# Performance work log

Hardware: AMD Instinct MI355X
Metric: run time of the kernel (lower is better)

Reference implementation:

```python
import jax, jax.numpy as jnp
import numpy as np

DT = 0.01
EPS = 1e-5


def setup_inputs() -> dict:
    key = jax.random.key(0)
    ks = jax.random.split(key, 20)
    B, H, IN, COV, CH, OH, OUT = 1024, 64, 8, 16, 64, 128, 2
    NE, OPE = 400, 256            # events, observations per event
    TOT = NE * OPE

    def w(k, sh, sc=0.05):
        return jax.random.normal(k, sh, dtype=jnp.float32) * sc

    return {
        'time_uniq': jnp.arange(NE, dtype=jnp.float32) * DT,   # event k fires at grid step k
        'time_ptr': jnp.arange(NE + 1, dtype=jnp.int32) * OPE,  # uniform obs per event
        'X': jax.random.normal(ks[0], (TOT, IN), dtype=jnp.float32),
        'sample_ids': jax.random.randint(ks[1], (TOT,), 0, B, dtype=jnp.int32),
        'covs': jax.random.normal(ks[2], (B, COV), dtype=jnp.float32),
        'T': 5,
        'cov_W1': w(ks[3], (CH, COV)), 'cov_b1': jnp.zeros((CH,), jnp.float32),
        'cov_W2': w(ks[4], (H, CH)),   'cov_b2': jnp.zeros((H,), jnp.float32),
        'gb_Wih': w(ks[5], (3 * H, IN)), 'gb_Whh': w(ks[6], (3 * H, H)),
        'gb_bih': jnp.zeros((3 * H,), jnp.float32), 'gb_bhh': jnp.zeros((3 * H,), jnp.float32),
        'gx_W': w(ks[7], (3 * H, 1)), 'gx_b': jnp.zeros((3 * H,), jnp.float32),
        'ghr_W': w(ks[8], (H, H)), 'ghz_W': w(ks[9], (H, H)), 'ghh_W': w(ks[10], (H, H)),
        'out_W1': w(ks[11], (OH, H)), 'out_b1': jnp.zeros((OH,), jnp.float32),
        'out_W2': w(ks[12], (OUT, OH)), 'out_b2': jnp.zeros((OUT,), jnp.float32),
    }


def _forward(time_uniq, time_ptr, X, sample_ids, covs, T,
             cov_W1, cov_b1, cov_W2, cov_b2,
             gb_Wih, gb_Whh, gb_bih, gb_bhh,
             gx_W, gx_b, ghr_W, ghz_W, ghh_W,
             out_W1, out_b1, out_W2, out_b2):
    n_events = time_uniq.shape[0]
    ope = X.shape[0] // n_events          # uniform observations per event (static)
    n_steps = int(round(T / DT))
    delta_t = DT

    # covariates_map (dropout p=0 -> identity)
    h0 = jnp.tanh(jnp.maximum(covs @ cov_W1.T + cov_b1, 0.0) @ cov_W2.T + cov_b2)

    def gru_bayes(x, h):                  # torch.nn.GRUCell semantics (gates r,z,n)
        gi = x @ gb_Wih.T + gb_bih
        gh = h @ gb_Whh.T + gb_bhh
        ir, iz, inn = jnp.split(gi, 3, axis=1)
        hr, hz, hn = jnp.split(gh, 3, axis=1)
        r = jax.nn.sigmoid(ir + hr)
        z = jax.nn.sigmoid(iz + hz)
        n = jnp.tanh(inn + r * hn)
        return (1.0 - z) * n + z * h

    def gru_ode(h):                       # FullGRUODECell with x = zeros
        px = jnp.zeros((h.shape[0], 1), h.dtype)
        gx = px @ gx_W.T + gx_b
        xr, xz, xh = jnp.split(gx, 3, axis=1)
        r = jax.nn.sigmoid(xr + h @ ghr_W.T)
        z = jax.nn.sigmoid(xz + h @ ghz_W.T)
        u = jnp.tanh(xh + (r * h) @ ghh_W.T)
        return h + delta_t * (1.0 - z) * (u - h)

    times = jnp.arange(n_steps, dtype=jnp.float32) * DT
    offs = jnp.arange(ope)

    def step(carry, t):
        h, i = carry
        ic = jnp.minimum(i, n_events - 1)
        fire = (i < n_events) & (time_uniq[ic] <= t + EPS)   # <=1 event per grid step
        obs = time_ptr[ic] + offs
        idx = sample_ids[obs]
        h_upd = h.at[idx].set(gru_bayes(X[obs], h[idx]))
        h = jnp.where(fire, h_upd, h)
        i = i + fire.astype(i.dtype)
        h_rec = h                          # recorded after events, before ODE step
        h = gru_ode(h)
        return (h, i), h_rec

    (h_last, _), h_steps = jax.lax.scan(step, (h0, jnp.int32(0)), times)
    h_path = jnp.concatenate([h_steps, h_last[None]], axis=0)   # [n_steps+1, B, H]

    # net_out (dropout p=0 -> identity)
    o = jnp.maximum(jnp.einsum('tbh,oh->tbo', h_path, out_W1) + out_b1, 0.0)
    return jnp.einsum('tbh,oh->tbo', o, out_W2) + out_b2


def reference(time_uniq, time_ptr, X, sample_ids, covs, T,
              cov_W1, cov_b1, cov_W2, cov_b2,
              gb_Wih, gb_Whh, gb_bih, gb_bhh,
              gx_W, gx_b, ghr_W, ghz_W, ghh_W,
              out_W1, out_b1, out_W2, out_b2):
    return _forward(time_uniq, time_ptr, X, sample_ids, covs, T,
                    cov_W1, cov_b1, cov_W2, cov_b2,
                    gb_Wih, gb_Whh, gb_bih, gb_bhh,
                    gx_W, gx_b, ghr_W, ghz_W, ghh_W,
                    out_W1, out_b1, out_W2, out_b2)
```

## Files before the change

### kernel.cpp

```cpp
#include <hip/hip_runtime.h>

#define DT_F 0.01f
#define EPS_F 1e-5f
#define NEG_INF_I (-1073741824)
#define NEC 1024

typedef _Float16 f16;
typedef _Float16 f16x2 __attribute__((ext_vector_type(2)));
typedef _Float16 f16x8 __attribute__((ext_vector_type(8)));
typedef float f32x4 __attribute__((ext_vector_type(4)));

#define MFMA16(a, b, c) __builtin_amdgcn_mfma_f32_16x16x32_f16((a), (b), (c), 0, 0, 0)

__device__ __forceinline__ float rl(float v, int l) {
  return __int_as_float(__builtin_amdgcn_readlane(__float_as_int(v), l));
}
__device__ __forceinline__ float sigm(float x) {
  float e = __builtin_amdgcn_exp2f(-1.442695041f * x);
  return __builtin_amdgcn_rcpf(1.0f + e);
}
__device__ __forceinline__ float tanhf_fast(float x) {
  float e = __builtin_amdgcn_exp2f(2.885390082f * x);
  return fmaf(-2.0f, __builtin_amdgcn_rcpf(e + 1.0f), 1.0f);
}
__device__ __forceinline__ float dot2(unsigned w, unsigned h, float acc) {
  return __builtin_amdgcn_fdot2(__builtin_bit_cast(f16x2, w),
                                __builtin_bit_cast(f16x2, h), acc, false);
}
__device__ __forceinline__ unsigned packf16(float a, float b) {
  return __builtin_bit_cast(unsigned, __builtin_amdgcn_cvt_pkrtz(a, b));
}
#define ANCH4(v) asm volatile("" : "+v"((v).x), "+v"((v).y), "+v"((v).z), "+v"((v).w))

__global__ void build_evtab_kernel(const int* __restrict__ sample_ids,
                                   const int* __restrict__ time_ptr,
                                   int* __restrict__ evtabT, int B, int ope) {
  int k = blockIdx.x;
  int base = time_ptr[k];
  for (int t = threadIdx.x; t < ope; t += blockDim.x) {
    int obs = base + t;
    int sid = sample_ids[obs];
    atomicMax(&evtabT[(long)sid * NEC + k], obs + 1);
  }
}

__global__ void pack_pairs_kernel(const float* __restrict__ ghr,
                                  const float* __restrict__ ghz,
                                  const float* __restrict__ ghh,
                                  const float* __restrict__ gbWhh,
                                  const float* __restrict__ gbWih,
                                  unsigned* __restrict__ odeP,
                                  unsigned* __restrict__ bayP,
                                  unsigned* __restrict__ wihP, int IN) {
  int idx = blockIdx.x * 256 + threadIdx.x;
  if (idx < 3 * 64 * 32) {
    int p = idx & 31, r = idx >> 5;
    int g = r >> 6, i = r & 63;
    const float* src = (g == 0) ? ghr : ((g == 1) ? ghz : ghh);
    odeP[idx] = packf16(src[i * 64 + 2 * p], src[i * 64 + 2 * p + 1]);
    bayP[idx] = packf16(gbWhh[r * 64 + 2 * p], gbWhh[r * 64 + 2 * p + 1]);
  }
  if (idx < 3 * 64 * 4) {
    int p = idx & 3, r = idx >> 2;
    float a = (2 * p < IN) ? gbWih[r * IN + 2 * p] : 0.0f;
    float b = (2 * p + 1 < IN) ? gbWih[r * IN + 2 * p + 1] : 0.0f;
    wihP[idx] = packf16(a, b);
  }
}

__global__ void pack_head_kernel(const float* __restrict__ W1, f16* __restrict__ w1P) {
  int f = blockIdx.x;
  int l = threadIdx.x;
  int t = f >> 1, kf = f & 1;
  int n = 16 * t + (l & 15);
  for (int j = 0; j < 8; ++j) {
    int k = 8 * (l >> 4) + j + 32 * kf;
    w1P[f * 512 + l * 8 + j] = (f16)W1[n * 64 + k];
  }
}

__global__ __launch_bounds__(128, 2) void evolve_kernel(
    const float* __restrict__ time_uniq,
    const float* __restrict__ X,
    const float* __restrict__ covs,
    const float* __restrict__ cov_W1, const float* __restrict__ cov_b1,
    const float* __restrict__ cov_W2, const float* __restrict__ cov_b2,
    const float* __restrict__ gb_bih, const float* __restrict__ gb_bhh,
    const float* __restrict__ gx_b,
    const unsigned* __restrict__ odeP, const unsigned* __restrict__ bayP,
    const unsigned* __restrict__ wihP,
    const int* __restrict__ evtabT,
    f16* __restrict__ hp16,
    int B, int NE, int n_steps, int IN, int COV)
{
  __shared__ unsigned sBW[3 * 64 * 32];
  __shared__ int sStep[1024];
  __shared__ int sEvt[1024];
  __shared__ __align__(16) f16 sHimg[64];
  __shared__ __align__(16) f16 sRHimg[64];

  const int tid = threadIdx.x;
  const int wid = tid >> 6, lane = tid & 63;
  const int b = blockIdx.x;
  const int necap = (NE < NEC) ? NE : NEC;

  for (int idx = tid; idx < 3 * 64 * 32; idx += 128) {
    int c = idx & 31, r = idx >> 5;
    int i = r & 63, s = c >> 2;
    sBW[r * 32 + (((s ^ (i & 7)) << 2) | (c & 3))] = bayP[idx];
  }
  for (int e = tid; e < necap; e += 128)
    sEvt[e] = evtabT[(long)b * NEC + e];
  if (wid == 0) {
    int pm = NEG_INF_I;
    int loc[16];
#pragma unroll
    for (int j = 0; j < 16; ++j) {
      int e = lane * 16 + j;
      int gv = NEG_INF_I;
      if (e < necap) {
        float tu = time_uniq[e];
        int k0 = (int)floorf((tu - EPS_F) * 100.0f) - 2;
        if (k0 < 0) k0 = 0;
        while ((float)k0 * DT_F + EPS_F < tu) ++k0;
        gv = k0 - e;
      }
      pm = max(pm, gv);
      loc[j] = pm;
    }
    int tot = pm;
#pragma unroll
    for (int off = 1; off < 64; off <<= 1) {
      int v = __shfl_up(tot, off);
      if (lane >= off) tot = max(tot, v);
    }
    int excl = __shfl_up(tot, 1);
    if (lane == 0) excl = NEG_INF_I;
#pragma unroll
    for (int j = 0; j < 16; ++j)
      sStep[lane * 16 + j] = lane * 16 + j + max(loc[j], excl);
  }
  if (wid == 0) {
    float cacc = cov_b1[lane];
    for (int c = 0; c < COV; ++c)
      cacc = fmaf(covs[b * COV + c], cov_W1[lane * COV + c], cacc);
    float cl = fmaxf(cacc, 0.0f);
    float hacc = cov_b2[lane];
#pragma unroll
    for (int j = 0; j < 64; ++j)
      hacc = fmaf(rl(cl, j), cov_W2[lane * 64 + j], hacc);
    sHimg[lane] = (f16)tanhf_fast(hacc);
  }
  __syncthreads();

  const uint4* odeQ = (const uint4*)odeP;
  const uint4* hq4 = (const uint4*)sHimg;
  const uint4* rq4 = (const uint4*)sRHimg;

  if (wid == 0) {
    uint4 WZ[8], WU[8];
#pragma unroll
    for (int q = 0; q < 8; ++q) {
      WZ[q] = odeQ[(1 * 64 + lane) * 8 + q];
      WU[q] = odeQ[(2 * 64 + lane) * 8 + q];
    }
#pragma unroll
    for (int q = 0; q < 8; ++q) { ANCH4(WZ[q]); ANCH4(WU[q]); }
    const uint4* wihQ = (const uint4*)wihP;

    const float xz = gx_b[64 + lane], xh = gx_b[128 + lane];
    const float crz_r = gb_bih[lane] + gb_bhh[lane];
    const float crz_z = gb_bih[64 + lane] + gb_bhh[64 + lane];
    const float bihn = gb_bih[128 + lane], bhhn = gb_bhh[128 + lane];

    float h = (float)sHimg[lane];

    int e_next = 0, s_next = 0x7fffffff, v_cur = 0, v_pipe = 0;
    float xf[8];
#pragma unroll
    for (int kk = 0; kk < 8; ++kk) xf[kk] = 0.0f;
    if (necap > 0) {
      s_next = sStep[0];
      v_cur = sEvt[0];
      if (v_cur > 0) {
        const float* xp = X + (long)(v_cur - 1) * IN;
#pragma unroll
        for (int kk = 0; kk < 8; ++kk) xf[kk] = (kk < IN) ? xp[kk] : 0.0f;
      }
      v_pipe = (necap > 1) ? sEvt[1] : 0;
    }

#pragma unroll 1
    for (int k = 0; k < n_steps; ++k) {
      if (k == s_next) {
        const bool fire = (v_cur > 0);
        if (fire) {
          unsigned xp0 = packf16(xf[0], xf[1]), xp1 = packf16(xf[2], xf[3]);
          unsigned xp2 = packf16(xf[4], xf[5]), xp3 = packf16(xf[6], xf[7]);
          uint4 wxr = wihQ[lane], wxz = wihQ[64 + lane], wxn = wihQ[128 + lane];
          float ar = crz_r, az = crz_z, anh = bhhn, ani = bihn;
          ar = dot2(wxr.x, xp0, ar); ar = dot2(wxr.y, xp1, ar);
          ar = dot2(wxr.z, xp2, ar); ar = dot2(wxr.w, xp3, ar);
          az = dot2(wxz.x, xp0, az); az = dot2(wxz.y, xp1, az);
          az = dot2(wxz.z, xp2, az); az = dot2(wxz.w, xp3, az);
          ani = dot2(wxn.x, xp0, ani); ani = dot2(wxn.y, xp1, ani);
          ani = dot2(wxn.z, xp2, ani); ani = dot2(wxn.w, xp3, ani);
          float ar1 = 0.f, az1 = 0.f, an1 = 0.f;
#pragma unroll
          for (int q = 0; q < 8; ++q) {
            uint4 hh = hq4[q];
            int sw = ((q ^ (lane & 7)) << 2);
            uint4 br = *(const uint4*)&sBW[(0 * 64 + lane) * 32 + sw];
            uint4 bz = *(const uint4*)&sBW[(1 * 64 + lane) * 32 + sw];
            uint4 bn = *(const uint4*)&sBW[(2 * 64 + lane) * 32 + sw];
            ar  = dot2(br.x, hh.x, ar);   ar1 = dot2(br.y, hh.y, ar1);
            ar  = dot2(br.z, hh.z, ar);   ar1 = dot2(br.w, hh.w, ar1);
            az  = dot2(bz.x, hh.x, az);   az1 = dot2(bz.y, hh.y, az1);
            az  = dot2(bz.z, hh.z, az);   az1 = dot2(bz.w, hh.w, az1);
            anh = dot2(bn.x, hh.x, anh);  an1 = dot2(bn.y, hh.y, an1);
            anh = dot2(bn.z, hh.z, anh);  an1 = dot2(bn.w, hh.w, an1);
          }
          float r = sigm(ar + ar1);
          float z = sigm(az + az1);
          float n = tanhf_fast(ani + r * (anh + an1));
          h = (1.0f - z) * n + z * h;
          sHimg[lane] = (f16)h;
        }
        ++e_next;
        if (e_next < necap) {
          s_next = sStep[e_next];
          v_cur = v_pipe;
          if (v_cur > 0) {
            const float* xp = X + (long)(v_cur - 1) * IN;
#pragma unroll
            for (int kk = 0; kk < 8; ++kk) xf[kk] = (kk < IN) ? xp[kk] : 0.0f;
          }
          v_pipe = (e_next + 1 < necap) ? sEvt[e_next + 1] : 0;
        } else {
          s_next = 0x7fffffff;
          v_cur = 0;
        }
        if (fire) __syncthreads();
      }

      float az0 = xz, az1 = 0.f, az2 = 0.f, az3 = 0.f;
#pragma unroll
      for (int q = 0; q < 8; ++q) {
        uint4 hp = hq4[q];
        az0 = dot2(WZ[q].x, hp.x, az0); az1 = dot2(WZ[q].y, hp.y, az1);
        az2 = dot2(WZ[q].z, hp.z, az2); az3 = dot2(WZ[q].w, hp.w, az3);
      }
      float z = sigm((az0 + az1) + (az2 + az3));
      __syncthreads();

      float au0 = xh, au1 = 0.f, au2 = 0.f, au3 = 0.f;
#pragma unroll
      for (int q = 0; q < 8; ++q) {
        uint4 rp = rq4[q];
        au0 = dot2(WU[q].x, rp.x, au0); au1 = dot2(WU[q].y, rp.y, au1);
        au2 = dot2(WU[q].z, rp.z, au2); au3 = dot2(WU[q].w, rp.w, au3);
      }
      float u = tanhf_fast((au0 + au1) + (au2 + au3));
      h = fmaf(DT_F * (1.0f - z), u - h, h);
      sHimg[lane] = (f16)h;
      __syncthreads();
    }
  } else {
    uint4 WR[8];
#pragma unroll
    for (int q = 0; q < 8; ++q) WR[q] = odeQ[(0 * 64 + lane) * 8 + q];
#pragma unroll
    for (int q = 0; q < 8; ++q) ANCH4(WR[q]);
    const float xr = gx_b[lane];

    f16* hps = hp16 + (long)b * 64 + lane;
    const long rowstride = (long)B * 64;

    int e_next = 0, s_next = 0x7fffffff, v_cur = 0, v_pipe = 0;
    if (necap > 0) {
      s_next = sStep[0];
      v_cur = sEvt[0];
      v_pipe = (necap > 1) ? sEvt[1] : 0;
    }

#pragma unroll 1
    for (int k = 0; k < n_steps; ++k) {
      if (k == s_next) {
        const bool fire = (v_cur > 0);
        ++e_next;
        if (e_next < necap) {
          s_next = sStep[e_next];
          v_cur = v_pipe;
          v_pipe = (e_next + 1 < necap) ? sEvt[e_next + 1] : 0;
        } else {
          s_next = 0x7fffffff;
          v_cur = 0;
        }
        if (fire) __syncthreads();
      }

      f16 hraw = sHimg[lane];
      *hps = hraw;
      hps += rowstride;
      float hf = (float)hraw;

      float ar0 = xr, ar1 = 0.f, ar2 = 0.f, ar3 = 0.f;
#pragma unroll
      for (int q = 0; q < 8; ++q) {
        uint4 hp = hq4[q];
        ar0 = dot2(WR[q].x, hp.x, ar0); ar1 = dot2(WR[q].y, hp.y, ar1);
        ar2 = dot2(WR[q].z, hp.z, ar2); ar3 = dot2(WR[q].w, hp.w, ar3);
      }
      float r = sigm((ar0 + ar1) + (ar2 + ar3));
      sRHimg[lane] = (f16)(r * hf);
      __syncthreads();
      __syncthreads();
    }
    *hps = sHimg[lane];
  }
}

__global__ __launch_bounds__(256, 4) void head_mfma_kernel(
    const f16* __restrict__ hp16, const f16* __restrict__ w1P,
    const float* __restrict__ b1, const float* __restrict__ W2,
    const float* __restrict__ b2, float* __restrict__ out, long nrows)
{
  const int wq = threadIdx.x >> 6, lane = threadIdx.x & 63;
  const int col = lane & 15;
  const long rowbase = ((long)blockIdx.x * 4 + wq) * 64;

  f16x8 Wf[8][2];
#pragma unroll
  for (int t = 0; t < 8; ++t)
#pragma unroll
    for (int kf = 0; kf < 2; ++kf)
      Wf[t][kf] = ((const f16x8*)w1P)[(2 * t + kf) * 64 + lane];

  float b1v[8], w2a[8], w2b[8];
#pragma unroll
  for (int t = 0; t < 8; ++t) {
    b1v[t] = b1[16 * t + col];
    w2a[t] = W2[16 * t + col];
    w2b[t] = W2[128 + 16 * t + col];
  }
  const float b20 = b2[0], b21 = b2[1];

#pragma unroll 1
  for (int g = 0; g < 4; ++g) {
    long row0 = rowbase + g * 16;
    long arow = row0 + col;
    f16x8 aH0 = {0, 0, 0, 0, 0, 0, 0, 0}, aH1 = aH0;
    if (arow < nrows) {
      const f16x8* ap = (const f16x8*)(hp16 + arow * 64);
      aH0 = ap[lane >> 4];
      aH1 = ap[(lane >> 4) + 4];
    }
    float p0[4] = {0.f, 0.f, 0.f, 0.f}, p1[4] = {0.f, 0.f, 0.f, 0.f};
#pragma unroll
    for (int t = 0; t < 8; ++t) {
      f32x4 c = {0.f, 0.f, 0.f, 0.f};
      c = MFMA16(aH0, Wf[t][0], c);
      c = MFMA16(aH1, Wf[t][1], c);
#pragma unroll
      for (int i = 0; i < 4; ++i) {
        float o = fmaxf(c[i] + b1v[t], 0.0f);
        p0[i] = fmaf(o, w2a[t], p0[i]);
        p1[i] = fmaf(o, w2b[t], p1[i]);
      }
    }
#pragma unroll
    for (int off = 1; off < 16; off <<= 1) {
#pragma unroll
      for (int i = 0; i < 4; ++i) {
        p0[i] += __shfl_xor(p0[i], off);
        p1[i] += __shfl_xor(p1[i], off);
      }
    }
    if (col == 0) {
#pragma unroll
      for (int i = 0; i < 4; ++i) {
        long row = row0 + (lane >> 4) * 4 + i;
        if (row < nrows) {
          out[row * 2 + 0] = p0[i] + b20;
          out[row * 2 + 1] = p1[i] + b21;
        }
      }
    }
  }
}

extern "C" void kernel_launch(void* const* d_in, const int* in_sizes, int n_in,
                              void* d_out, int out_size, void* d_ws, size_t ws_size,
                              hipStream_t stream) {
  const float* time_uniq  = (const float*)d_in[0];
  const int*   time_ptr   = (const int*)d_in[1];
  const float* X          = (const float*)d_in[2];
  const int*   sample_ids = (const int*)d_in[3];
  const float* covs       = (const float*)d_in[4];
  const float* cov_W1     = (const float*)d_in[6];
  const float* cov_b1     = (const float*)d_in[7];
  const float* cov_W2     = (const float*)d_in[8];
  const float* cov_b2     = (const float*)d_in[9];
  const float* gb_Wih     = (const float*)d_in[10];
  const float* gb_Whh     = (const float*)d_in[11];
  const float* gb_bih     = (const float*)d_in[12];
  const float* gb_bhh     = (const float*)d_in[13];
  const float* gx_b       = (const float*)d_in[15];
  const float* ghr_W      = (const float*)d_in[16];
  const float* ghz_W      = (const float*)d_in[17];
  const float* ghh_W      = (const float*)d_in[18];
  const float* out_W1     = (const float*)d_in[19];
  const float* out_b1     = (const float*)d_in[20];
  const float* out_W2     = (const float*)d_in[21];
  const float* out_b2     = (const float*)d_in[22];

  int NE   = in_sizes[0];
  int TOT  = in_sizes[3];
  int IN   = in_sizes[2] / TOT;
  int CH   = in_sizes[7];
  int COV  = in_sizes[6] / CH;
  int B    = in_sizes[4] / COV;
  int OUTD = in_sizes[22];
  int n_steps = out_size / (B * OUTD) - 1;
  int OPE  = TOT / NE;

  char* ws = (char*)d_ws;
  int* evtabT = (int*)ws;
  size_t evbytes = (size_t)B * NEC * sizeof(int);
  size_t off1 = (evbytes + 255) & ~(size_t)255;
  unsigned* odeP = (unsigned*)(ws + off1);
  unsigned* bayP = odeP + 3 * 64 * 32;
  unsigned* wihP = bayP + 3 * 64 * 32;
  size_t off2 = off1 + (((3 * 64 * 32 * 2 + 3 * 64 * 4) * sizeof(unsigned) + 255) & ~(size_t)255);
  f16* w1P = (f16*)(ws + off2);
  size_t off3 = off2 + ((16 * 512 * sizeof(f16) + 255) & ~(size_t)255);
  f16* hp16 = (f16*)(ws + off3);

  hipMemsetAsync(evtabT, 0, evbytes, stream);
  build_evtab_kernel<<<NE, 256, 0, stream>>>(sample_ids, time_ptr, evtabT, B, OPE);
  pack_pairs_kernel<<<24, 256, 0, stream>>>(ghr_W, ghz_W, ghh_W, gb_Whh, gb_Wih,
                                            odeP, bayP, wihP, IN);
  pack_head_kernel<<<16, 64, 0, stream>>>(out_W1, w1P);
  evolve_kernel<<<B, 128, 0, stream>>>(
      time_uniq, X, covs, cov_W1, cov_b1, cov_W2, cov_b2,
      gb_bih, gb_bhh, gx_b, odeP, bayP, wihP,
      evtabT, hp16, B, NE, n_steps, IN, COV);
  long nrows = (long)(n_steps + 1) * B;
  int hb = (int)((nrows + 255) / 256);
  head_mfma_kernel<<<hb, 256, 0, stream>>>(hp16, w1P, out_b1, out_W2, out_b2,
                                           (float*)d_out, nrows);
}
```

Measured before the change: 432.5 us.

## Move reset gate onto main wave and offload update gate to helper wave

Wave 0 now computes the ODE reset gate and r*h itself, then runs the candidate matvec straight away. Because the write to sRHimg and the read that follows happen in the same wavefront, no cross-wave barrier is needed between them. The update gate z moves to the helper wave and is passed back through a new shared array, so it is off the serial r→u dependency chain. The hidden-state vector is also kept in registers (hpre) after each update instead of being reloaded from LDS, and wave 0 raises its scheduling priority. One side effect is that r*h now uses the fp32 h rather than its f16-rounded value, which slightly changes the numerics.

```diff
diff --git a/kernel.cpp b/kernel.cpp
--- a/kernel.cpp
+++ b/kernel.cpp
@@ -98,6 +98,7 @@
   __shared__ int sEvt[1024];
   __shared__ __align__(16) f16 sHimg[64];
   __shared__ __align__(16) f16 sRHimg[64];
+  __shared__ float sZ[64];
 
   const int tid = threadIdx.x;
   const int wid = tid >> 6, lane = tid & 63;
@@ -158,22 +159,26 @@
   const uint4* rq4 = (const uint4*)sRHimg;
 
   if (wid == 0) {
-    uint4 WZ[8], WU[8];
+    __builtin_amdgcn_s_setprio(1);
+    uint4 WR[8], WU[8];
 #pragma unroll
     for (int q = 0; q < 8; ++q) {
-      WZ[q] = odeQ[(1 * 64 + lane) * 8 + q];
+      WR[q] = odeQ[(0 * 64 + lane) * 8 + q];
       WU[q] = odeQ[(2 * 64 + lane) * 8 + q];
     }
 #pragma unroll
-    for (int q = 0; q < 8; ++q) { ANCH4(WZ[q]); ANCH4(WU[q]); }
+    for (int q = 0; q < 8; ++q) { ANCH4(WR[q]); ANCH4(WU[q]); }
     const uint4* wihQ = (const uint4*)wihP;
 
-    const float xz = gx_b[64 + lane], xh = gx_b[128 + lane];
+    const float xr = gx_b[lane], xh = gx_b[128 + lane];
     const float crz_r = gb_bih[lane] + gb_bhh[lane];
     const float crz_z = gb_bih[64 + lane] + gb_bhh[64 + lane];
     const float bihn = gb_bih[128 + lane], bhhn = gb_bhh[128 + lane];
 
     float h = (float)sHimg[lane];
+    uint4 hpre[8];
+#pragma unroll
+    for (int q = 0; q < 8; ++q) hpre[q] = hq4[q];
 
     int e_next = 0, s_next = 0x7fffffff, v_cur = 0, v_pipe = 0;
     float xf[8];
@@ -208,23 +213,24 @@
           float ar1 = 0.f, az1 = 0.f, an1 = 0.f;
 #pragma unroll
           for (int q = 0; q < 8; ++q) {
-            uint4 hh = hq4[q];
             int sw = ((q ^ (lane & 7)) << 2);
             uint4 br = *(const uint4*)&sBW[(0 * 64 + lane) * 32 + sw];
             uint4 bz = *(const uint4*)&sBW[(1 * 64 + lane) * 32 + sw];
             uint4 bn = *(const uint4*)&sBW[(2 * 64 + lane) * 32 + sw];
-            ar  = dot2(br.x, hh.x, ar);   ar1 = dot2(br.y, hh.y, ar1);
-            ar  = dot2(br.z, hh.z, ar);   ar1 = dot2(br.w, hh.w, ar1);
-            az  = dot2(bz.x, hh.x, az);   az1 = dot2(bz.y, hh.y, az1);
-            az  = dot2(bz.z, hh.z, az);   az1 = dot2(bz.w, hh.w, az1);
-            anh = dot2(bn.x, hh.x, anh);  an1 = dot2(bn.y, hh.y, an1);
-            anh = dot2(bn.z, hh.z, anh);  an1 = dot2(bn.w, hh.w, an1);
+            ar  = dot2(br.x, hpre[q].x, ar);   ar1 = dot2(br.y, hpre[q].y, ar1);
+            ar  = dot2(br.z, hpre[q].z, ar);   ar1 = dot2(br.w, hpre[q].w, ar1);
+            az  = dot2(bz.x, hpre[q].x, az);   az1 = dot2(bz.y, hpre[q].y, az1);
+            az  = dot2(bz.z, hpre[q].z, az);   az1 = dot2(bz.w, hpre[q].w, az1);
+            anh = dot2(bn.x, hpre[q].x, anh);  an1 = dot2(bn.y, hpre[q].y, an1);
+            anh = dot2(bn.z, hpre[q].z, anh);  an1 = dot2(bn.w, hpre[q].w, an1);
           }
           float r = sigm(ar + ar1);
           float z = sigm(az + az1);
           float n = tanhf_fast(ani + r * (anh + an1));
           h = (1.0f - z) * n + z * h;
           sHimg[lane] = (f16)h;
+#pragma unroll
+          for (int q = 0; q < 8; ++q) hpre[q] = hq4[q];
         }
         ++e_next;
         if (e_next < necap) {
@@ -243,16 +249,15 @@
         if (fire) __syncthreads();
       }
 
-      float az0 = xz, az1 = 0.f, az2 = 0.f, az3 = 0.f;
+      float ar0 = xr, ar1 = 0.f, ar2 = 0.f, ar3 = 0.f;
 #pragma unroll
       for (int q = 0; q < 8; ++q) {
-        uint4 hp = hq4[q];
-        az0 = dot2(WZ[q].x, hp.x, az0); az1 = dot2(WZ[q].y, hp.y, az1);
-        az2 = dot2(WZ[q].z, hp.z, az2); az3 = dot2(WZ[q].w, hp.w, az3);
-      }
-      float z = sigm((az0 + az1) + (az2 + az3));
-      __syncthreads();
-
+        ar0 = dot2(WR[q].x, hpre[q].x, ar0); ar1 = dot2(WR[q].y, hpre[q].y, ar1);
+        ar2 = dot2(WR[q].z, hpre[q].z, ar2); ar3 = dot2(WR[q].w, hpre[q].w, ar3);
+      }
+      float r = sigm((ar0 + ar1) + (ar2 + ar3));
+
+      sRHimg[lane] = (f16)(r * h);
       float au0 = xh, au1 = 0.f, au2 = 0.f, au3 = 0.f;
 #pragma unroll
       for (int q = 0; q < 8; ++q) {
@@ -260,18 +265,22 @@
         au0 = dot2(WU[q].x, rp.x, au0); au1 = dot2(WU[q].y, rp.y, au1);
         au2 = dot2(WU[q].z, rp.z, au2); au3 = dot2(WU[q].w, rp.w, au3);
       }
+      __syncthreads();
+      float zv = sZ[lane];
       float u = tanhf_fast((au0 + au1) + (au2 + au3));
-      h = fmaf(DT_F * (1.0f - z), u - h, h);
+      h = fmaf(DT_F * (1.0f - zv), u - h, h);
       sHimg[lane] = (f16)h;
+#pragma unroll
+      for (int q = 0; q < 8; ++q) hpre[q] = hq4[q];
       __syncthreads();
     }
   } else {
-    uint4 WR[8];
-#pragma unroll
-    for (int q = 0; q < 8; ++q) WR[q] = odeQ[(0 * 64 + lane) * 8 + q];
-#pragma unroll
-    for (int q = 0; q < 8; ++q) ANCH4(WR[q]);
-    const float xr = gx_b[lane];
+    uint4 WZ[8];
+#pragma unroll
+    for (int q = 0; q < 8; ++q) WZ[q] = odeQ[(1 * 64 + lane) * 8 + q];
+#pragma unroll
+    for (int q = 0; q < 8; ++q) ANCH4(WZ[q]);
+    const float xz = gx_b[64 + lane];
 
     f16* hps = hp16 + (long)b * 64 + lane;
     const long rowstride = (long)B * 64;
@@ -302,17 +311,15 @@
       f16 hraw = sHimg[lane];
       *hps = hraw;
       hps += rowstride;
-      float hf = (float)hraw;
-
-      float ar0 = xr, ar1 = 0.f, ar2 = 0.f, ar3 = 0.f;
+
+      float az0 = xz, az1 = 0.f, az2 = 0.f, az3 = 0.f;
 #pragma unroll
       for (int q = 0; q < 8; ++q) {
-        uint4 hp = hq4[q];
-        ar0 = dot2(WR[q].x, hp.x, ar0); ar1 = dot2(WR[q].y, hp.y, ar1);
-        ar2 = dot2(WR[q].z, hp.z, ar2); ar3 = dot2(WR[q].w, hp.w, ar3);
-      }
-      float r = sigm((ar0 + ar1) + (ar2 + ar3));
-      sRHimg[lane] = (f16)(r * hf);
+        uint4 hh = hq4[q];
+        az0 = dot2(WZ[q].x, hh.x, az0); az1 = dot2(WZ[q].y, hh.y, az1);
+        az2 = dot2(WZ[q].z, hh.z, az2); az3 = dot2(WZ[q].w, hh.w, az3);
+      }
+      sZ[lane] = sigm((az0 + az1) + (az2 + az3));
       __syncthreads();
       __syncthreads();
     }
```

Result: slower. 441.2 us (+2.0%).
